# Kernel tuning notes

Hardware: AMD Instinct MI355X
Metric: run time of the kernel (lower is better)

The kernel has to match this reference:

```python
import jax, jax.numpy as jnp
import numpy as np
from jax import lax

UNITS = 64
LAYERS = 4

def _lstm_layer(x, Wx, U, b):
    # x: [B,T,F]; Keras gate order i,f,c,o; activation=relu, recurrent_activation=sigmoid
    B = x.shape[0]
    xz = jnp.einsum('btf,fg->btg', x, Wx) + b  # precompute input projections [B,T,4U]
    def step(carry, xz_t):
        h, c = carry
        z = xz_t + h @ U
        i, f, g, o = jnp.split(z, 4, axis=-1)
        c = jax.nn.sigmoid(f) * c + jax.nn.sigmoid(i) * jax.nn.relu(g)
        h = jax.nn.sigmoid(o) * jax.nn.relu(c)
        return (h, c), h
    h0 = jnp.zeros((B, UNITS), dtype=x.dtype)
    c0 = jnp.zeros((B, UNITS), dtype=x.dtype)
    _, hs = lax.scan(step, (h0, c0), jnp.swapaxes(xz, 0, 1))
    return jnp.swapaxes(hs, 0, 1)  # [B,T,U]

def setup_inputs() -> dict:
    key = jax.random.key(0)
    ks = jax.random.split(key, 1 + 3 * LAYERS + 2)
    B, T, F = 1024, 512, 1
    d = {'x': jax.random.normal(ks[0], (B, T, F), dtype=jnp.float32)}
    fin = F
    for l in range(LAYERS):
        d[f'Wx{l}'] = jax.random.normal(ks[1 + 3 * l], (fin, 4 * UNITS), dtype=jnp.float32) * 0.05
        d[f'U{l}'] = jax.random.normal(ks[2 + 3 * l], (UNITS, 4 * UNITS), dtype=jnp.float32) * 0.05
        d[f'b{l}'] = jnp.zeros((4 * UNITS,), dtype=jnp.float32)
        fin = UNITS
    d['Wd'] = jax.random.normal(ks[-2], (UNITS, 1), dtype=jnp.float32) * 0.05
    d['bd'] = jnp.zeros((1,), dtype=jnp.float32)
    return d

def reference(x, Wx0, U0, b0, Wx1, U1, b1, Wx2, U2, b2, Wx3, U3, b3, Wd, bd):
    # Dropout is identity at inference.
    h = x
    for Wx, U, b in ((Wx0, U0, b0), (Wx1, U1, b1), (Wx2, U2, b2), (Wx3, U3, b3)):
        h = _lstm_layer(h, Wx, U, b)
    h_last = h[:, -1, :]  # return_sequences=False on last LSTM
    return h_last @ Wd + bd  # [B,1]
```

## Files before the change

kernel.cpp:

```cpp
#include <hip/hip_runtime.h>
#include <stdint.h>

#define TT 512

typedef __fp16   f16x8  __attribute__((ext_vector_type(8)));
typedef float    f32x4  __attribute__((ext_vector_type(4)));
typedef __fp16   fp16x2 __attribute__((ext_vector_type(2)));
typedef uint32_t u32x2  __attribute__((ext_vector_type(2)));

__device__ __forceinline__ f32x4 mfma16(f16x8 a, f16x8 b, f32x4 c) {
    return __builtin_amdgcn_mfma_f32_16x16x32_f16(a, b, c, 0, 0, 0);
}
__device__ __forceinline__ uint32_t pkf16(float a, float b) {
    fp16x2 h = __builtin_amdgcn_cvt_pkrtz(a, b);
    return __builtin_bit_cast(uint32_t, h);
}

#define REP8(M) M(0)M(1)M(2)M(3)M(4)M(5)M(6)M(7)

#define GA(SRC, T, F) (f16x8){ \
  (__fp16)(SRC)[(32*(F)+8*quad+0)*256 + 16*(T)+l15], \
  (__fp16)(SRC)[(32*(F)+8*quad+1)*256 + 16*(T)+l15], \
  (__fp16)(SRC)[(32*(F)+8*quad+2)*256 + 16*(T)+l15], \
  (__fp16)(SRC)[(32*(F)+8*quad+3)*256 + 16*(T)+l15], \
  (__fp16)(SRC)[(32*(F)+8*quad+4)*256 + 16*(T)+l15], \
  (__fp16)(SRC)[(32*(F)+8*quad+5)*256 + 16*(T)+l15], \
  (__fp16)(SRC)[(32*(F)+8*quad+6)*256 + 16*(T)+l15], \
  (__fp16)(SRC)[(32*(F)+8*quad+7)*256 + 16*(T)+l15] }

#define DECLT(j) f16x8 uA##j##_0, uA##j##_1, wA##j##_0, wA##j##_1; f32x4 bias##j;
#define LOADT(j) { \
  const int Tg_ = ((j)>>1)*4 + 2*h + ((j)&1); \
  uA##j##_0 = GA(Uw, Tg_, 0); uA##j##_1 = GA(Uw, Tg_, 1); \
  bias##j = (f32x4){ bw_[16*Tg_ + 4*quad + 0], bw_[16*Tg_ + 4*quad + 1], \
                     bw_[16*Tg_ + 4*quad + 2], bw_[16*Tg_ + 4*quad + 3] }; \
  if (l > 0) { wA##j##_0 = GA(Wsrc, Tg_, 0); wA##j##_1 = GA(Wsrc, Tg_, 1); } \
  else { wA##j##_0 = __builtin_bit_cast(f16x8, (f32x4){ \
           Wx0[16*Tg_+4*quad+0], Wx0[16*Tg_+4*quad+1], \
           Wx0[16*Tg_+4*quad+2], Wx0[16*Tg_+4*quad+3] }); \
         wA##j##_1 = wA##j##_0; } }

#define MW0(j) acc##j = mfma16(wA##j##_0, xBp0, bias##j);
#define MW1(j) acc##j = mfma16(wA##j##_1, xBp1, acc##j);
#define MX(j)  acc##j = bias##j + __builtin_bit_cast(f32x4, wA##j##_0) * xvp4;
#define MU0(j) acc##j = mfma16(uA##j##_0, hB0, acc##j);
#define MU1(j) acc##j = mfma16(uA##j##_1, hB1, acc##j);

#define MFMA_SEG(t_) { \
  const __fp16* hp_ = hb_l + (((t_)-1)&7)*1152 + l15*72 + 8*quad; \
  f16x8 hB0 = *(const f16x8*)hp_; \
  f16x8 hB1 = *(const f16x8*)(hp_ + 32); \
  if (l > 0) { REP8(MW0) REP8(MW1) } \
  else       { f32x4 xvp4 = {xvp, xvp, xvp, xvp}; REP8(MX) } \
  REP8(MU0) \
  REP8(MU1) }

#define GATES(qp, Ai, Af, Ag, Ao, CST, SAVEK, HK) { \
  f32x4 ei_, ef_, eo_; \
  _Pragma("unroll") for (int r_ = 0; r_ < 4; ++r_) { \
    ei_[r_] = __builtin_amdgcn_exp2f(-1.4426950408889634f * Ai[r_]); \
    ef_[r_] = __builtin_amdgcn_exp2f(-1.4426950408889634f * Af[r_]); \
    eo_[r_] = __builtin_amdgcn_exp2f(-1.4426950408889634f * Ao[r_]); \
  } \
  f32x4 si_, sf_, so_; \
  _Pragma("unroll") for (int r_ = 0; r_ < 4; ++r_) { \
    si_[r_] = __builtin_amdgcn_rcpf(1.0f + ei_[r_]); \
    sf_[r_] = __builtin_amdgcn_rcpf(1.0f + ef_[r_]); \
    so_[r_] = __builtin_amdgcn_rcpf(1.0f + eo_[r_]); \
  } \
  const f32x4 z4_ = {0.f, 0.f, 0.f, 0.f}; \
  f32x4 rg_ = __builtin_elementwise_max(Ag, z4_); \
  f32x4 cv_ = sf_ * CST + si_ * rg_; \
  CST = cv_; \
  f32x4 hv_ = so_ * __builtin_elementwise_max(cv_, z4_); \
  u32x2 pv_ = { pkf16(hv_[0], hv_[1]), pkf16(hv_[2], hv_[3]) }; \
  *(u32x2*)(hw_ + 16*(qp)) = pv_; \
  if (SAVEK) HK = hv_; }

#define GATE_SEG(tg_, SV_) { \
  __fp16* hw_ = hb_l + ((tg_)&7)*1152 + l15*72 + 32*h + 4*quad; \
  GATES(0, acc0, acc2, acc4, acc6, cst0, SV_, hK0) \
  GATES(1, acc1, acc3, acc5, acc7, cst1, SV_, hK1) }

#define WAITGE(cache, idx, need) \
  while ((cache) < (need)) \
    (cache) = __hip_atomic_load(&Pf[idx], __ATOMIC_ACQUIRE, __HIP_MEMORY_SCOPE_WORKGROUP);

__global__ __launch_bounds__(512)
__attribute__((amdgpu_waves_per_eu(2, 2)))
void lstm_phase(
    const float* __restrict__ x,
    const float* __restrict__ Wx0, const float* __restrict__ U0, const float* __restrict__ b0,
    const float* __restrict__ Wx1, const float* __restrict__ U1, const float* __restrict__ b1,
    const float* __restrict__ Wx2, const float* __restrict__ U2, const float* __restrict__ b2,
    const float* __restrict__ Wx3, const float* __restrict__ U3, const float* __restrict__ b3,
    const float* __restrict__ Wd,  const float* __restrict__ bd,
    float* __restrict__ out)
{
    extern __shared__ uint32_t smem[];
    __fp16* hb16 = (__fp16*)smem;
    float*  xs   = (float*)(smem + 18432);
    float*  red  = (float*)(smem + 27136);
    int*    Pf   = (int*)(smem + 27168);

    const int tid  = threadIdx.x;
    const int lane = tid & 63;
    const int l15  = lane & 15;
    const int quad = lane >> 4;
    const int wv   = tid >> 6;
    const int l    = wv >> 1;
    const int h    = wv & 1;
    const int b0i  = blockIdx.x * 16;

    for (int i = tid; i < 27176; i += 512) smem[i] = 0;
    __syncthreads();
    for (int i = tid; i < 16 * TT; i += 512) {
        int row = i >> 9, t_ = i & (TT - 1);
        xs[t_ * 17 + row] = x[(b0i + row) * TT + t_];
    }

    const float* Uw   = (l == 0) ? U0 : (l == 1) ? U1 : (l == 2) ? U2 : U3;
    const float* bw_  = (l == 0) ? b0 : (l == 1) ? b1 : (l == 2) ? b2 : b3;
    const float* Wsrc = (l == 1) ? Wx1 : (l == 2) ? Wx2 : (l == 3) ? Wx3 : U0;

    REP8(DECLT)
    REP8(LOADT)

    f32x4 acc0, acc1, acc2, acc3, acc4, acc5, acc6, acc7;
    f32x4 cst0 = {0,0,0,0}, cst1 = {0,0,0,0};
    f32x4 hK0  = {0,0,0,0}, hK1  = {0,0,0,0};

    __fp16* hb_l  = hb16 + l * 9216;
    const __fp16* hb_in = hb16 + (l > 0 ? (l - 1) * 9216 : 0);

    f16x8 xBp0 = {}, xBp1 = {};
    float xvp = 0.f;

    __syncthreads();

    if (l == 0) xvp = xs[l15];

    int pA0 = 0, pA1 = 0, pP = 0, pC0 = 0, pC1 = 0;

    for (int t = 0; t < TT; ++t) {
        if (l > 0) {
            WAITGE(pA0, 2*l - 2, t + 1)
            WAITGE(pA1, 2*l - 1, t + 1)
            const __fp16* xp_ = hb_in + (t & 7) * 1152 + l15 * 72 + 8 * quad;
            xBp0 = *(const f16x8*)xp_;
            xBp1 = *(const f16x8*)(xp_ + 32);
        }
        if (t > 0) WAITGE(pP, 2*l + 1 - h, t)
        if (l < 3 && t >= 8) {
            WAITGE(pC0, 2*l + 2, t - 7)
            WAITGE(pC1, 2*l + 3, t - 7)
        }
        MFMA_SEG(t)
        {
            const bool sv_ = (l == 3) && (t == TT - 1);
            GATE_SEG(t, sv_)
        }
        __hip_atomic_store(&Pf[2*l + h], t + 1, __ATOMIC_RELEASE, __HIP_MEMORY_SCOPE_WORKGROUP);
        if (l == 0 && t + 1 < TT) xvp = xs[(t + 1) * 17 + l15];
    }

    __syncthreads();

    if (l == 3) {
        float p = 0.f;
        #pragma unroll
        for (int r = 0; r < 4; ++r) {
            p += hK0[r] * Wd[32 * h + 4 * quad + r];
            p += hK1[r] * Wd[32 * h + 16 + 4 * quad + r];
        }
        p += __shfl_down(p, 32, 64);
        p += __shfl_down(p, 16, 64);
        if (lane < 16) red[h * 16 + lane] = p;
    }
    __syncthreads();
    if (wv == 6 && lane < 16) out[b0i + lane] = red[lane] + red[16 + lane] + bd[0];
}

extern "C" void kernel_launch(void* const* d_in, const int* in_sizes, int n_in,
                              void* d_out, int out_size, void* d_ws, size_t ws_size,
                              hipStream_t stream) {
    const float* x   = (const float*)d_in[0];
    const float* Wx0 = (const float*)d_in[1];
    const float* U0  = (const float*)d_in[2];
    const float* b0  = (const float*)d_in[3];
    const float* Wx1 = (const float*)d_in[4];
    const float* U1  = (const float*)d_in[5];
    const float* b1  = (const float*)d_in[6];
    const float* Wx2 = (const float*)d_in[7];
    const float* U2  = (const float*)d_in[8];
    const float* b2  = (const float*)d_in[9];
    const float* Wx3 = (const float*)d_in[10];
    const float* U3  = (const float*)d_in[11];
    const float* b3  = (const float*)d_in[12];
    const float* Wd  = (const float*)d_in[13];
    const float* bd  = (const float*)d_in[14];
    float* out = (float*)d_out;

    static const int kLds = 27176 * 4;
    (void)hipFuncSetAttribute((const void*)lstm_phase,
                              hipFuncAttributeMaxDynamicSharedMemorySize, kLds);
    hipLaunchKernelGGL(lstm_phase, dim3(64), dim3(512), kLds, stream,
                       x, Wx0, U0, b0, Wx1, U1, b1, Wx2, U2, b2, Wx3, U3, b3,
                       Wd, bd, out);
}
```

Baseline: 648.8 us.

## Give each LSTM layer to a single wave that owns all gate columns

Each layer is now computed by one wave instead of two, so the wave holds all 64 hidden units and feeds its own h straight back into the next step's MFMA operand in registers. This removes the per-step intra-layer handshake through LDS. The gate columns are permuted so the MFMA output layout matches the B-operand layout. Biases and Wx0 are staged in LDS instead of registers. In exchange each wave runs twice the MFMAs per step and holds far more weight registers (waves_per_eu 1), which lengthens the serial critical path per timestep.

Measured after the change: 1.205 ms. 1.86x slower.

```diff
diff --git a/kernel.cpp b/kernel.cpp
--- a/kernel.cpp
+++ b/kernel.cpp
@@ -6,7 +6,7 @@
 typedef __fp16   f16x8  __attribute__((ext_vector_type(8)));
 typedef float    f32x4  __attribute__((ext_vector_type(4)));
 typedef __fp16   fp16x2 __attribute__((ext_vector_type(2)));
-typedef uint32_t u32x2  __attribute__((ext_vector_type(2)));
+typedef uint32_t u32x4  __attribute__((ext_vector_type(4)));
 
 __device__ __forceinline__ f32x4 mfma16(f16x8 a, f16x8 b, f32x4 c) {
     return __builtin_amdgcn_mfma_f32_16x16x32_f16(a, b, c, 0, 0, 0);
@@ -16,79 +16,13 @@
     return __builtin_bit_cast(uint32_t, h);
 }
 
-#define REP8(M) M(0)M(1)M(2)M(3)M(4)M(5)M(6)M(7)
-
-#define GA(SRC, T, F) (f16x8){ \
-  (__fp16)(SRC)[(32*(F)+8*quad+0)*256 + 16*(T)+l15], \
-  (__fp16)(SRC)[(32*(F)+8*quad+1)*256 + 16*(T)+l15], \
-  (__fp16)(SRC)[(32*(F)+8*quad+2)*256 + 16*(T)+l15], \
-  (__fp16)(SRC)[(32*(F)+8*quad+3)*256 + 16*(T)+l15], \
-  (__fp16)(SRC)[(32*(F)+8*quad+4)*256 + 16*(T)+l15], \
-  (__fp16)(SRC)[(32*(F)+8*quad+5)*256 + 16*(T)+l15], \
-  (__fp16)(SRC)[(32*(F)+8*quad+6)*256 + 16*(T)+l15], \
-  (__fp16)(SRC)[(32*(F)+8*quad+7)*256 + 16*(T)+l15] }
-
-#define DECLT(j) f16x8 uA##j##_0, uA##j##_1, wA##j##_0, wA##j##_1; f32x4 bias##j;
-#define LOADT(j) { \
-  const int Tg_ = ((j)>>1)*4 + 2*h + ((j)&1); \
-  uA##j##_0 = GA(Uw, Tg_, 0); uA##j##_1 = GA(Uw, Tg_, 1); \
-  bias##j = (f32x4){ bw_[16*Tg_ + 4*quad + 0], bw_[16*Tg_ + 4*quad + 1], \
-                     bw_[16*Tg_ + 4*quad + 2], bw_[16*Tg_ + 4*quad + 3] }; \
-  if (l > 0) { wA##j##_0 = GA(Wsrc, Tg_, 0); wA##j##_1 = GA(Wsrc, Tg_, 1); } \
-  else { wA##j##_0 = __builtin_bit_cast(f16x8, (f32x4){ \
-           Wx0[16*Tg_+4*quad+0], Wx0[16*Tg_+4*quad+1], \
-           Wx0[16*Tg_+4*quad+2], Wx0[16*Tg_+4*quad+3] }); \
-         wA##j##_1 = wA##j##_0; } }
-
-#define MW0(j) acc##j = mfma16(wA##j##_0, xBp0, bias##j);
-#define MW1(j) acc##j = mfma16(wA##j##_1, xBp1, acc##j);
-#define MX(j)  acc##j = bias##j + __builtin_bit_cast(f32x4, wA##j##_0) * xvp4;
-#define MU0(j) acc##j = mfma16(uA##j##_0, hB0, acc##j);
-#define MU1(j) acc##j = mfma16(uA##j##_1, hB1, acc##j);
-
-#define MFMA_SEG(t_) { \
-  const __fp16* hp_ = hb_l + (((t_)-1)&7)*1152 + l15*72 + 8*quad; \
-  f16x8 hB0 = *(const f16x8*)hp_; \
-  f16x8 hB1 = *(const f16x8*)(hp_ + 32); \
-  if (l > 0) { REP8(MW0) REP8(MW1) } \
-  else       { f32x4 xvp4 = {xvp, xvp, xvp, xvp}; REP8(MX) } \
-  REP8(MU0) \
-  REP8(MU1) }
-
-#define GATES(qp, Ai, Af, Ag, Ao, CST, SAVEK, HK) { \
-  f32x4 ei_, ef_, eo_; \
-  _Pragma("unroll") for (int r_ = 0; r_ < 4; ++r_) { \
-    ei_[r_] = __builtin_amdgcn_exp2f(-1.4426950408889634f * Ai[r_]); \
-    ef_[r_] = __builtin_amdgcn_exp2f(-1.4426950408889634f * Af[r_]); \
-    eo_[r_] = __builtin_amdgcn_exp2f(-1.4426950408889634f * Ao[r_]); \
-  } \
-  f32x4 si_, sf_, so_; \
-  _Pragma("unroll") for (int r_ = 0; r_ < 4; ++r_) { \
-    si_[r_] = __builtin_amdgcn_rcpf(1.0f + ei_[r_]); \
-    sf_[r_] = __builtin_amdgcn_rcpf(1.0f + ef_[r_]); \
-    so_[r_] = __builtin_amdgcn_rcpf(1.0f + eo_[r_]); \
-  } \
-  const f32x4 z4_ = {0.f, 0.f, 0.f, 0.f}; \
-  f32x4 rg_ = __builtin_elementwise_max(Ag, z4_); \
-  f32x4 cv_ = sf_ * CST + si_ * rg_; \
-  CST = cv_; \
-  f32x4 hv_ = so_ * __builtin_elementwise_max(cv_, z4_); \
-  u32x2 pv_ = { pkf16(hv_[0], hv_[1]), pkf16(hv_[2], hv_[3]) }; \
-  *(u32x2*)(hw_ + 16*(qp)) = pv_; \
-  if (SAVEK) HK = hv_; }
-
-#define GATE_SEG(tg_, SV_) { \
-  __fp16* hw_ = hb_l + ((tg_)&7)*1152 + l15*72 + 32*h + 4*quad; \
-  GATES(0, acc0, acc2, acc4, acc6, cst0, SV_, hK0) \
-  GATES(1, acc1, acc3, acc5, acc7, cst1, SV_, hK1) }
-
 #define WAITGE(cache, idx, need) \
   while ((cache) < (need)) \
     (cache) = __hip_atomic_load(&Pf[idx], __ATOMIC_ACQUIRE, __HIP_MEMORY_SCOPE_WORKGROUP);
 
-__global__ __launch_bounds__(512)
-__attribute__((amdgpu_waves_per_eu(2, 2)))
-void lstm_phase(
+__global__ __launch_bounds__(256)
+__attribute__((amdgpu_waves_per_eu(1, 1)))
+void lstm_owner(
     const float* __restrict__ x,
     const float* __restrict__ Wx0, const float* __restrict__ U0, const float* __restrict__ b0,
     const float* __restrict__ Wx1, const float* __restrict__ U1, const float* __restrict__ b1,
@@ -98,87 +32,164 @@
     float* __restrict__ out)
 {
     extern __shared__ uint32_t smem[];
-    __fp16* hb16 = (__fp16*)smem;
-    float*  xs   = (float*)(smem + 18432);
-    float*  red  = (float*)(smem + 27136);
-    int*    Pf   = (int*)(smem + 27168);
+    __fp16* ring = (__fp16*)smem;
+    float*  xs   = (float*)(smem + 12288);
+    float*  bs   = (float*)(smem + 20992);
+    float*  wxs  = (float*)(smem + 22016);
+    int*    Pf   = (int*)(smem + 22272);
 
     const int tid  = threadIdx.x;
     const int lane = tid & 63;
     const int l15  = lane & 15;
     const int quad = lane >> 4;
-    const int wv   = tid >> 6;
-    const int l    = wv >> 1;
-    const int h    = wv & 1;
+    const int l    = tid >> 6;
     const int b0i  = blockIdx.x * 16;
 
-    for (int i = tid; i < 27176; i += 512) smem[i] = 0;
-    __syncthreads();
-    for (int i = tid; i < 16 * TT; i += 512) {
+    for (int i = tid; i < 16 * TT; i += 256) {
         int row = i >> 9, t_ = i & (TT - 1);
         xs[t_ * 17 + row] = x[(b0i + row) * TT + t_];
     }
+    for (int i = tid; i < 1024; i += 256) {
+        const float* bsrc = (i < 256) ? b0 : (i < 512) ? b1 : (i < 768) ? b2 : b3;
+        bs[i] = bsrc[i & 255];
+    }
+    wxs[tid] = Wx0[tid];
+    if (tid < 4) Pf[tid] = 0;
 
     const float* Uw   = (l == 0) ? U0 : (l == 1) ? U1 : (l == 2) ? U2 : U3;
-    const float* bw_  = (l == 0) ? b0 : (l == 1) ? b1 : (l == 2) ? b2 : b3;
     const float* Wsrc = (l == 1) ? Wx1 : (l == 2) ? Wx2 : (l == 3) ? Wx3 : U0;
 
-    REP8(DECLT)
-    REP8(LOADT)
-
-    f32x4 acc0, acc1, acc2, acc3, acc4, acc5, acc6, acc7;
-    f32x4 cst0 = {0,0,0,0}, cst1 = {0,0,0,0};
-    f32x4 hK0  = {0,0,0,0}, hK1  = {0,0,0,0};
-
-    __fp16* hb_l  = hb16 + l * 9216;
-    const __fp16* hb_in = hb16 + (l > 0 ? (l - 1) * 9216 : 0);
-
-    f16x8 xBp0 = {}, xBp1 = {};
-    float xvp = 0.f;
+    f16x8 uA[4][4][2];
+    f16x8 wA[4][4][2];
+    #pragma unroll
+    for (int G = 0; G < 4; ++G)
+      #pragma unroll
+      for (int g = 0; g < 4; ++g) {
+        const int zc = 64*g + 32*(G>>1) + 8*(l15>>2) + 4*(G&1) + (l15&3);
+        #pragma unroll
+        for (int F = 0; F < 2; ++F) {
+          f16x8 v;
+          #pragma unroll
+          for (int j = 0; j < 8; ++j) v[j] = (__fp16)Uw[(32*F + 8*quad + j)*256 + zc];
+          uA[G][g][F] = v;
+          if (l > 0) {
+            f16x8 w2;
+            #pragma unroll
+            for (int j = 0; j < 8; ++j) w2[j] = (__fp16)Wsrc[(32*F + 8*quad + j)*256 + zc];
+            wA[G][g][F] = w2;
+          }
+        }
+      }
+
+    f32x4 acc[4][4];
+    f32x4 cst[4] = {};
+    f32x4 hs[4]  = {};
+    f16x8 hB0 = {}, hB1 = {};
+    f16x8 xB0 = {}, xB1 = {};
+
+    __fp16*       rout = ring + l * 8192;
+    const __fp16* rin  = ring + (l - 1) * 8192;
+    const float*  bsl  = bs + l * 256;
 
     __syncthreads();
 
-    if (l == 0) xvp = xs[l15];
-
-    int pA0 = 0, pA1 = 0, pP = 0, pC0 = 0, pC1 = 0;
+    int pIn = 0, pOut = 0;
 
     for (int t = 0; t < TT; ++t) {
+        float xvp = 0.f;
+        if (l == 0) {
+            xvp = xs[t * 17 + l15];
+        } else {
+            WAITGE(pIn, l - 1, t + 1)
+            const __fp16* rp = rin + (t & 7) * 1024 + lane * 8;
+            xB0 = *(const f16x8*)rp;
+            xB1 = *(const f16x8*)(rp + 512);
+        }
+        if (l < 3 && t >= 8) WAITGE(pOut, l + 1, t - 7)
+
+        #pragma unroll
+        for (int G = 0; G < 4; ++G)
+          #pragma unroll
+          for (int g = 0; g < 4; ++g) {
+            const int bo = 64*g + 32*(G>>1) + 8*quad + 4*(G&1);
+            f32x4 bv = *(const f32x4*)(bsl + bo);
+            if (l == 0) {
+                f32x4 wv = *(const f32x4*)(wxs + bo);
+                acc[G][g] = bv + wv * xvp;
+            } else {
+                acc[G][g] = mfma16(wA[G][g][0], xB0, bv);
+            }
+          }
         if (l > 0) {
-            WAITGE(pA0, 2*l - 2, t + 1)
-            WAITGE(pA1, 2*l - 1, t + 1)
-            const __fp16* xp_ = hb_in + (t & 7) * 1152 + l15 * 72 + 8 * quad;
-            xBp0 = *(const f16x8*)xp_;
-            xBp1 = *(const f16x8*)(xp_ + 32);
-        }
-        if (t > 0) WAITGE(pP, 2*l + 1 - h, t)
-        if (l < 3 && t >= 8) {
-            WAITGE(pC0, 2*l + 2, t - 7)
-            WAITGE(pC1, 2*l + 3, t - 7)
-        }
-        MFMA_SEG(t)
-        {
-            const bool sv_ = (l == 3) && (t == TT - 1);
-            GATE_SEG(t, sv_)
-        }
-        __hip_atomic_store(&Pf[2*l + h], t + 1, __ATOMIC_RELEASE, __HIP_MEMORY_SCOPE_WORKGROUP);
-        if (l == 0 && t + 1 < TT) xvp = xs[(t + 1) * 17 + l15];
-    }
-
-    __syncthreads();
+          #pragma unroll
+          for (int G = 0; G < 4; ++G)
+            #pragma unroll
+            for (int g = 0; g < 4; ++g)
+              acc[G][g] = mfma16(wA[G][g][1], xB1, acc[G][g]);
+        }
+        #pragma unroll
+        for (int G = 0; G < 4; ++G)
+          #pragma unroll
+          for (int g = 0; g < 4; ++g)
+            acc[G][g] = mfma16(uA[G][g][0], hB0, acc[G][g]);
+        #pragma unroll
+        for (int G = 0; G < 4; ++G)
+          #pragma unroll
+          for (int g = 0; g < 4; ++g)
+            acc[G][g] = mfma16(uA[G][g][1], hB1, acc[G][g]);
+
+        uint32_t w[8];
+        const bool sv = (l == 3) && (t == TT - 1);
+        #pragma unroll
+        for (int G = 0; G < 4; ++G) {
+            f32x4 Ai = acc[G][0], Af = acc[G][1], Ag = acc[G][2], Ao = acc[G][3];
+            f32x4 ei, ef, eo;
+            #pragma unroll
+            for (int r = 0; r < 4; ++r) {
+                ei[r] = __builtin_amdgcn_exp2f(-1.4426950408889634f * Ai[r]);
+                ef[r] = __builtin_amdgcn_exp2f(-1.4426950408889634f * Af[r]);
+                eo[r] = __builtin_amdgcn_exp2f(-1.4426950408889634f * Ao[r]);
+            }
+            f32x4 si, sf, so;
+            #pragma unroll
+            for (int r = 0; r < 4; ++r) {
+                si[r] = __builtin_amdgcn_rcpf(1.0f + ei[r]);
+                sf[r] = __builtin_amdgcn_rcpf(1.0f + ef[r]);
+                so[r] = __builtin_amdgcn_rcpf(1.0f + eo[r]);
+            }
+            const f32x4 z4 = {0.f, 0.f, 0.f, 0.f};
+            f32x4 rg = __builtin_elementwise_max(Ag, z4);
+            f32x4 cv = sf * cst[G] + si * rg;
+            cst[G] = cv;
+            f32x4 hv = so * __builtin_elementwise_max(cv, z4);
+            w[2*G + 0] = pkf16(hv[0], hv[1]);
+            w[2*G + 1] = pkf16(hv[2], hv[3]);
+            if (sv) hs[G] = hv;
+        }
+        u32x4 f0 = {w[0], w[1], w[2], w[3]};
+        u32x4 f1 = {w[4], w[5], w[6], w[7]};
+        hB0 = __builtin_bit_cast(f16x8, f0);
+        hB1 = __builtin_bit_cast(f16x8, f1);
+        if (l < 3) {
+            __fp16* wp = rout + (t & 7) * 1024 + lane * 8;
+            *(u32x4*)wp = f0;
+            *(u32x4*)(wp + 512) = f1;
+        }
+        __hip_atomic_store(&Pf[l], t + 1, __ATOMIC_RELEASE, __HIP_MEMORY_SCOPE_WORKGROUP);
+    }
 
     if (l == 3) {
         float p = 0.f;
         #pragma unroll
-        for (int r = 0; r < 4; ++r) {
-            p += hK0[r] * Wd[32 * h + 4 * quad + r];
-            p += hK1[r] * Wd[32 * h + 16 + 4 * quad + r];
+        for (int G = 0; G < 4; ++G) {
+            const int ub = 8*quad + 4*(G&1) + 32*(G>>1);
+            #pragma unroll
+            for (int r = 0; r < 4; ++r) p += hs[G][r] * Wd[ub + r];
         }
         p += __shfl_down(p, 32, 64);
         p += __shfl_down(p, 16, 64);
-        if (lane < 16) red[h * 16 + lane] = p;
-    }
-    __syncthreads();
-    if (wv == 6 && lane < 16) out[b0i + lane] = red[lane] + red[16 + lane] + bd[0];
+        if (lane < 16) out[b0i + lane] = p + bd[0];
+    }
 }
 
 extern "C" void kernel_launch(void* const* d_in, const int* in_sizes, int n_in,
@@ -201,10 +212,10 @@
     const float* bd  = (const float*)d_in[14];
     float* out = (float*)d_out;
 
-    static const int kLds = 27176 * 4;
-    (void)hipFuncSetAttribute((const void*)lstm_phase,
+    static const int kLds = 22276 * 4;
+    (void)hipFuncSetAttribute((const void*)lstm_owner,
                               hipFuncAttributeMaxDynamicSharedMemorySize, kLds);
-    hipLaunchKernelGGL(lstm_phase, dim3(64), dim3(512), kLds, stream,
+    hipLaunchKernelGGL(lstm_owner, dim3(64), dim3(256), kLds, stream,
                        x, Wx0, U0, b0, Wx1, U1, b1, Wx2, U2, b2, Wx3, U3, b3,
                        Wd, bd, out);
 }
```

## Precompute next-step input projection after gates and fold sigmoid scale into weights

Applied to the files above, without the earlier changes.

The input-projection MFMAs for step t+1 now run right after step t's gates and flag store, instead of on the critical path after waiting on the recurrent h. The recurrent MFMAs start from this precomputed accumulator. The -log2(e) factor for the sigmoid gates is folded into the weights and bias at load time, removing a multiply per exponent. s_setprio raises wave priority around the recurrent MFMA segment. In exchange, each wave now waits on the lower layer one step earlier and holds an extra set of accumulator registers. Scaling the weights before the fp16 conversion also changes rounding slightly.

New measurement: 823.9 us. 1.27x slower.

```diff
diff --git a/kernel.cpp b/kernel.cpp
--- a/kernel.cpp
+++ b/kernel.cpp
@@ -18,49 +18,50 @@
 
 #define REP8(M) M(0)M(1)M(2)M(3)M(4)M(5)M(6)M(7)
 
-#define GA(SRC, T, F) (f16x8){ \
-  (__fp16)(SRC)[(32*(F)+8*quad+0)*256 + 16*(T)+l15], \
-  (__fp16)(SRC)[(32*(F)+8*quad+1)*256 + 16*(T)+l15], \
-  (__fp16)(SRC)[(32*(F)+8*quad+2)*256 + 16*(T)+l15], \
-  (__fp16)(SRC)[(32*(F)+8*quad+3)*256 + 16*(T)+l15], \
-  (__fp16)(SRC)[(32*(F)+8*quad+4)*256 + 16*(T)+l15], \
-  (__fp16)(SRC)[(32*(F)+8*quad+5)*256 + 16*(T)+l15], \
-  (__fp16)(SRC)[(32*(F)+8*quad+6)*256 + 16*(T)+l15], \
-  (__fp16)(SRC)[(32*(F)+8*quad+7)*256 + 16*(T)+l15] }
+#define GA(SRC, T, F, SC) (f16x8){ \
+  (__fp16)((SRC)[(32*(F)+8*quad+0)*256 + 16*(T)+l15] * (SC)), \
+  (__fp16)((SRC)[(32*(F)+8*quad+1)*256 + 16*(T)+l15] * (SC)), \
+  (__fp16)((SRC)[(32*(F)+8*quad+2)*256 + 16*(T)+l15] * (SC)), \
+  (__fp16)((SRC)[(32*(F)+8*quad+3)*256 + 16*(T)+l15] * (SC)), \
+  (__fp16)((SRC)[(32*(F)+8*quad+4)*256 + 16*(T)+l15] * (SC)), \
+  (__fp16)((SRC)[(32*(F)+8*quad+5)*256 + 16*(T)+l15] * (SC)), \
+  (__fp16)((SRC)[(32*(F)+8*quad+6)*256 + 16*(T)+l15] * (SC)), \
+  (__fp16)((SRC)[(32*(F)+8*quad+7)*256 + 16*(T)+l15] * (SC)) }
 
 #define DECLT(j) f16x8 uA##j##_0, uA##j##_1, wA##j##_0, wA##j##_1; f32x4 bias##j;
 #define LOADT(j) { \
   const int Tg_ = ((j)>>1)*4 + 2*h + ((j)&1); \
-  uA##j##_0 = GA(Uw, Tg_, 0); uA##j##_1 = GA(Uw, Tg_, 1); \
-  bias##j = (f32x4){ bw_[16*Tg_ + 4*quad + 0], bw_[16*Tg_ + 4*quad + 1], \
-                     bw_[16*Tg_ + 4*quad + 2], bw_[16*Tg_ + 4*quad + 3] }; \
-  if (l > 0) { wA##j##_0 = GA(Wsrc, Tg_, 0); wA##j##_1 = GA(Wsrc, Tg_, 1); } \
+  const float sc_ = (((j)>>1) == 2) ? 1.0f : -1.4426950408889634f; \
+  uA##j##_0 = GA(Uw, Tg_, 0, sc_); uA##j##_1 = GA(Uw, Tg_, 1, sc_); \
+  bias##j = (f32x4){ bw_[16*Tg_ + 4*quad + 0] * sc_, bw_[16*Tg_ + 4*quad + 1] * sc_, \
+                     bw_[16*Tg_ + 4*quad + 2] * sc_, bw_[16*Tg_ + 4*quad + 3] * sc_ }; \
+  if (l > 0) { wA##j##_0 = GA(Wsrc, Tg_, 0, sc_); wA##j##_1 = GA(Wsrc, Tg_, 1, sc_); } \
   else { wA##j##_0 = __builtin_bit_cast(f16x8, (f32x4){ \
-           Wx0[16*Tg_+4*quad+0], Wx0[16*Tg_+4*quad+1], \
-           Wx0[16*Tg_+4*quad+2], Wx0[16*Tg_+4*quad+3] }); \
+           Wx0[16*Tg_+4*quad+0] * sc_, Wx0[16*Tg_+4*quad+1] * sc_, \
+           Wx0[16*Tg_+4*quad+2] * sc_, Wx0[16*Tg_+4*quad+3] * sc_ }); \
          wA##j##_1 = wA##j##_0; } }
 
-#define MW0(j) acc##j = mfma16(wA##j##_0, xBp0, bias##j);
-#define MW1(j) acc##j = mfma16(wA##j##_1, xBp1, acc##j);
-#define MX(j)  acc##j = bias##j + __builtin_bit_cast(f32x4, wA##j##_0) * xvp4;
-#define MU0(j) acc##j = mfma16(uA##j##_0, hB0, acc##j);
-#define MU1(j) acc##j = mfma16(uA##j##_1, hB1, acc##j);
+#define DECLW(j) f32x4 wacc##j;
+#define WPREP(j)  wacc##j = mfma16(wA##j##_0, xBp0, bias##j); \
+                  wacc##j = mfma16(wA##j##_1, xBp1, wacc##j);
+#define WPREPX(j) wacc##j = bias##j + __builtin_bit_cast(f32x4, wA##j##_0) * xvp4;
+
+#define MUA(j) acc##j = mfma16(uA##j##_0, hB0, wacc##j);
+#define MUB(j) acc##j = mfma16(uA##j##_1, hB1, acc##j);
 
 #define MFMA_SEG(t_) { \
   const __fp16* hp_ = hb_l + (((t_)-1)&7)*1152 + l15*72 + 8*quad; \
   f16x8 hB0 = *(const f16x8*)hp_; \
   f16x8 hB1 = *(const f16x8*)(hp_ + 32); \
-  if (l > 0) { REP8(MW0) REP8(MW1) } \
-  else       { f32x4 xvp4 = {xvp, xvp, xvp, xvp}; REP8(MX) } \
-  REP8(MU0) \
-  REP8(MU1) }
+  REP8(MUA) \
+  REP8(MUB) }
 
 #define GATES(qp, Ai, Af, Ag, Ao, CST, SAVEK, HK) { \
   f32x4 ei_, ef_, eo_; \
   _Pragma("unroll") for (int r_ = 0; r_ < 4; ++r_) { \
-    ei_[r_] = __builtin_amdgcn_exp2f(-1.4426950408889634f * Ai[r_]); \
-    ef_[r_] = __builtin_amdgcn_exp2f(-1.4426950408889634f * Af[r_]); \
-    eo_[r_] = __builtin_amdgcn_exp2f(-1.4426950408889634f * Ao[r_]); \
+    ei_[r_] = __builtin_amdgcn_exp2f(Ai[r_]); \
+    ef_[r_] = __builtin_amdgcn_exp2f(Af[r_]); \
+    eo_[r_] = __builtin_amdgcn_exp2f(Ao[r_]); \
   } \
   f32x4 si_, sf_, so_; \
   _Pragma("unroll") for (int r_ = 0; r_ < 4; ++r_) { \
@@ -125,6 +126,7 @@
 
     REP8(DECLT)
     REP8(LOADT)
+    REP8(DECLW)
 
     f32x4 acc0, acc1, acc2, acc3, acc4, acc5, acc6, acc7;
     f32x4 cst0 = {0,0,0,0}, cst1 = {0,0,0,0};
@@ -134,34 +136,53 @@
     const __fp16* hb_in = hb16 + (l > 0 ? (l - 1) * 9216 : 0);
 
     f16x8 xBp0 = {}, xBp1 = {};
-    float xvp = 0.f;
-
-    __syncthreads();
-
-    if (l == 0) xvp = xs[l15];
+
+    __syncthreads();
 
     int pA0 = 0, pA1 = 0, pP = 0, pC0 = 0, pC1 = 0;
 
+    if (l == 0) {
+        float xvp = xs[l15];
+        f32x4 xvp4 = {xvp, xvp, xvp, xvp};
+        REP8(WPREPX)
+    } else {
+        WAITGE(pA0, 2*l - 2, 1)
+        WAITGE(pA1, 2*l - 1, 1)
+        const __fp16* xp_ = hb_in + 0 * 1152 + l15 * 72 + 8 * quad;
+        xBp0 = *(const f16x8*)xp_;
+        xBp1 = *(const f16x8*)(xp_ + 32);
+        REP8(WPREP)
+    }
+
     for (int t = 0; t < TT; ++t) {
-        if (l > 0) {
-            WAITGE(pA0, 2*l - 2, t + 1)
-            WAITGE(pA1, 2*l - 1, t + 1)
-            const __fp16* xp_ = hb_in + (t & 7) * 1152 + l15 * 72 + 8 * quad;
-            xBp0 = *(const f16x8*)xp_;
-            xBp1 = *(const f16x8*)(xp_ + 32);
-        }
         if (t > 0) WAITGE(pP, 2*l + 1 - h, t)
         if (l < 3 && t >= 8) {
             WAITGE(pC0, 2*l + 2, t - 7)
             WAITGE(pC1, 2*l + 3, t - 7)
         }
+        __builtin_amdgcn_s_setprio(1);
         MFMA_SEG(t)
+        __builtin_amdgcn_s_setprio(0);
         {
             const bool sv_ = (l == 3) && (t == TT - 1);
             GATE_SEG(t, sv_)
         }
         __hip_atomic_store(&Pf[2*l + h], t + 1, __ATOMIC_RELEASE, __HIP_MEMORY_SCOPE_WORKGROUP);
-        if (l == 0 && t + 1 < TT) xvp = xs[(t + 1) * 17 + l15];
+
+        if (t + 1 < TT) {
+            if (l == 0) {
+                float xvp = xs[(t + 1) * 17 + l15];
+                f32x4 xvp4 = {xvp, xvp, xvp, xvp};
+                REP8(WPREPX)
+            } else {
+                WAITGE(pA0, 2*l - 2, t + 2)
+                WAITGE(pA1, 2*l - 1, t + 2)
+                const __fp16* xp_ = hb_in + ((t + 1) & 7) * 1152 + l15 * 72 + 8 * quad;
+                xBp0 = *(const f16x8*)xp_;
+                xBp1 = *(const f16x8*)(xp_ + 32);
+                REP8(WPREP)
+            }
+        }
     }
 
     __syncthreads();
```
